# Kernel optimization log

Hardware: AMD Instinct MI355X
Metric: run time of the kernel (lower is better)

Reference implementation:

```python
import jax, jax.numpy as jnp
import numpy as np

GAMMA = 1.0 - 2.0 ** (-5)   # 0.96875, as in the module
NUM_GROUPS = 8
NUM_HEADS = 8
EPS = 1e-5


def setup_inputs() -> dict:
    key = jax.random.key(0)
    ks = jax.random.split(key, 8)
    M, S, Hd = 128, 512, 512  # num_segments, bonds per segment, hidden_size
    N = M * S
    return {
        "message": jax.random.normal(ks[0], (N, Hd), jnp.float32),
        "Wq": jax.random.normal(ks[1], (Hd, Hd), jnp.float32) / np.sqrt(Hd).astype(np.float32),
        "Wk": jax.random.normal(ks[2], (Hd, Hd), jnp.float32) / np.sqrt(Hd).astype(np.float32),
        "Wv": jax.random.normal(ks[3], (Hd, Hd), jnp.float32) / np.sqrt(Hd).astype(np.float32),
        "Wo": jax.random.normal(ks[4], (Hd, Hd), jnp.float32) / np.sqrt(Hd).astype(np.float32),
        "bo": jax.random.normal(ks[5], (Hd,), jnp.float32) * 0.01,
        "gn_w": jnp.ones((Hd,), jnp.float32),
        "gn_b": jnp.zeros((Hd,), jnp.float32),
        "num_segs": M,
        "seg_len": S,
    }


def _forward(message, Wq, Wk, Wv, Wo, bo, gn_w, gn_b, M, S):
    Hd = message.shape[1]
    H = NUM_HEADS
    d = Hd // H
    scale = jnp.float32(d ** (-0.5))
    gamma = jnp.float32(GAMMA)

    x = message.reshape(M, S, Hd)                       # equal contiguous segments
    q = (x @ Wq.T).reshape(M, S, H, d)
    k = (x @ Wk.T).reshape(M, S, H, d)
    v = (x @ Wv.T).reshape(M, S, H, d)

    # per-segment K^T V outer-product state contribution: [M, H, d, d]
    A = jnp.einsum('mshd,mshe->mhde', k, v)
    decay = gamma ** S  # gamma ** b_size for equal segments

    def step(r, a):
        # r = K_i^T V_i + gamma^{b_size} * r_prev  (state AFTER segment i, as in source)
        r_new = a + decay * r
        return r_new, r_new

    _, r_all = jax.lax.scan(step, jnp.zeros((H, d, d), x.dtype), A)  # [M, H, d, d]

    # intra-segment retention: (Q K^T) * scale @ V
    scores = jnp.einsum('mshd,mthd->mhst', q, k) * scale
    intra = jnp.einsum('mhst,mthd->mshd', scores, v)
    # cross/recurrent term: (Q @ r_i) * gamma^{i+1}  (note: NOT scaled by scale_factor)
    cross = jnp.einsum('mshd,mhde->mshe', q, r_all)
    g = (gamma ** jnp.arange(1, M + 1, dtype=jnp.float32))[:, None, None, None]
    h = jax.nn.relu(intra + cross * g)                  # activation; dropout p=0

    out = h.reshape(M, S, Hd) @ Wo.T + bo               # W_b_o
    res = x + out                                       # residual (dropout p=0)

    # GroupNorm(8, hidden): per segment (batch N=1), groups over hidden channels,
    # stats pooled over (hidden/8 group channels x S bonds)
    gsh = res.reshape(M, S, NUM_GROUPS, Hd // NUM_GROUPS)
    mean = gsh.mean(axis=(1, 3), keepdims=True)
    var = gsh.var(axis=(1, 3), keepdims=True)
    normed = ((gsh - mean) * jax.lax.rsqrt(var + EPS)).reshape(M, S, Hd)
    normed = normed * gn_w + gn_b

    flat = normed.reshape(M * S, Hd)
    # cached_zero_vector is prepended once before the first segment
    return jnp.concatenate([jnp.zeros((1, Hd), flat.dtype), flat], axis=0)


def reference(message, Wq, Wk, Wv, Wo, bo, gn_w, gn_b, num_segs, seg_len):
    return _forward(message, Wq, Wk, Wv, Wo, bo, gn_w, gn_b, num_segs, seg_len)
```

## Files before the change

kernel.cpp:

```cpp
#include <hip/hip_runtime.h>
#include <math.h>

#define M_SEG 128
#define S_SEG 512
#define HD 512
#define NHEAD 8
#define DHEAD 64
#define NROWS (M_SEG * S_SEG)
#define QKVLD 1536
#define GAMMA_F 0.96875f
#define SCALE_F 0.125f

typedef unsigned short u16;
typedef float f32x4 __attribute__((ext_vector_type(4)));
typedef __bf16 bf16x8 __attribute__((ext_vector_type(8)));
typedef unsigned short ushort8 __attribute__((ext_vector_type(8)));
typedef unsigned short ushort4v __attribute__((ext_vector_type(4)));

__device__ __forceinline__ u16 f2bf(float f) {
    union { float f; unsigned u; } x; x.f = f;
    unsigned r = x.u + 0x7FFFu + ((x.u >> 16) & 1u);
    return (u16)(r >> 16);
}
__device__ __forceinline__ float bf2f(u16 v) {
    union { unsigned u; float f; } x; x.u = ((unsigned)v) << 16;
    return x.f;
}

__device__ __forceinline__ void fence_all() {
    asm volatile("" ::: "memory");
    __builtin_amdgcn_sched_barrier(0);
}

__device__ __forceinline__ void gload16(const u16* g, u16* l) {
    __builtin_amdgcn_global_load_lds(
        (const __attribute__((address_space(1))) void*)g,
        (__attribute__((address_space(3))) void*)l, 16, 0, 0);
}

__global__ __launch_bounds__(256) void convert_bf16(const float* __restrict__ in,
                                                    u16* __restrict__ outp, int n8)
{
    int idx = blockIdx.x * 256 + threadIdx.x;
    if (idx >= n8) return;
    const float4 a = *reinterpret_cast<const float4*>(&in[(size_t)idx * 8]);
    const float4 b = *reinterpret_cast<const float4*>(&in[(size_t)idx * 8 + 4]);
    ushort8 o;
    o[0] = f2bf(a.x); o[1] = f2bf(a.y); o[2] = f2bf(a.z); o[3] = f2bf(a.w);
    o[4] = f2bf(b.x); o[5] = f2bf(b.y); o[6] = f2bf(b.z); o[7] = f2bf(b.w);
    *reinterpret_cast<ushort8*>(&outp[(size_t)idx * 8]) = o;
}

__global__ __launch_bounds__(256) void convert_weights(const float* __restrict__ w0,
                                                       const float* __restrict__ w1,
                                                       const float* __restrict__ w2,
                                                       const float* __restrict__ w3,
                                                       u16* __restrict__ outp)
{
    const int which = blockIdx.y;
    const float* src = which == 0 ? w0 : which == 1 ? w1 : which == 2 ? w2 : w3;
    u16* dst = outp + (size_t)which * 262144;
    int idx = blockIdx.x * 256 + threadIdx.x;
    const float4 a = *reinterpret_cast<const float4*>(&src[(size_t)idx * 8]);
    const float4 b = *reinterpret_cast<const float4*>(&src[(size_t)idx * 8 + 4]);
    ushort8 o;
    o[0] = f2bf(a.x); o[1] = f2bf(a.y); o[2] = f2bf(a.z); o[3] = f2bf(a.w);
    o[4] = f2bf(b.x); o[5] = f2bf(b.y); o[6] = f2bf(b.z); o[7] = f2bf(b.w);
    *reinterpret_cast<ushort8*>(&dst[(size_t)idx * 8]) = o;
}

template<int EPI>
__global__ __launch_bounds__(256, 4) void gemm4b(const u16* __restrict__ A, int lda,
                                                 const u16* __restrict__ B,
                                                 u16* __restrict__ Cv, int ldc, int ntile,
                                                 const u16* __restrict__ Xb,
                                                 const float* __restrict__ bias)
{
    __shared__ __align__(16) u16 sm[2][8192];
    const int t    = threadIdx.x;
    const int lane = t & 63;
    const int w    = t >> 6;
    const int wm   = w >> 1;
    const int wn   = w & 1;

    const int nwg  = gridDim.x;
    const int cpx  = nwg >> 3;
    const int bid  = blockIdx.x;
    const int sbid = (bid & 7) * cpx + (bid >> 3);
    const int mt = sbid / ntile, nt = sbid % ntile;
    const int rowBase = mt * 128, colBase = nt * 128;

    const int frow = lane & 15, fkc = lane >> 4, orow = (lane >> 4) * 4;

    const int sr0 = t >> 2;
    const int ksl = (t & 3) ^ ((sr0 >> 1) & 3);

    const size_t gA0 = (size_t)(rowBase + sr0)      * lda + ksl * 8;
    const size_t gA1 = (size_t)(rowBase + sr0 + 64) * lda + ksl * 8;
    const size_t gB0 = (size_t)(colBase + sr0)      * HD  + ksl * 8;
    const size_t gB1 = (size_t)(colBase + sr0 + 64) * HD  + ksl * 8;

    f32x4 acc[4][4];
#pragma unroll
    for (int i = 0; i < 4; ++i)
#pragma unroll
        for (int j = 0; j < 4; ++j)
            acc[i][j] = (f32x4){0.f, 0.f, 0.f, 0.f};

#define STAGE(kt, buf)                                                        \
    do {                                                                      \
        gload16(&A[gA0 + (kt) * 32], &sm[buf][t * 8]);                        \
        gload16(&A[gA1 + (kt) * 32], &sm[buf][2048 + t * 8]);                 \
        gload16(&B[gB0 + (kt) * 32], &sm[buf][4096 + t * 8]);                 \
        gload16(&B[gB1 + (kt) * 32], &sm[buf][6144 + t * 8]);                 \
    } while (0)

    STAGE(0, 0);
    STAGE(1, 1);

#pragma unroll 1
    for (int kt = 0; kt < 16; ++kt) {
        const int buf = kt & 1;
        if (kt < 15) asm volatile("s_waitcnt vmcnt(4)" ::: "memory");
        else         asm volatile("s_waitcnt vmcnt(0)" ::: "memory");
        __builtin_amdgcn_s_barrier();
        fence_all();

        const u16* Ab = sm[buf];
        const u16* Bb = sm[buf] + 4096;
        bf16x8 af[4], bfv[4];
#pragma unroll
        for (int mm = 0; mm < 4; ++mm) {
            const int r = wm * 64 + mm * 16 + frow;
            af[mm] = *reinterpret_cast<const bf16x8*>(
                &Ab[r * 32 + ((fkc ^ ((r >> 1) & 3)) << 3)]);
        }
#pragma unroll
        for (int nn = 0; nn < 4; ++nn) {
            const int r = wn * 64 + nn * 16 + frow;
            bfv[nn] = *reinterpret_cast<const bf16x8*>(
                &Bb[r * 32 + ((fkc ^ ((r >> 1) & 3)) << 3)]);
        }
        __builtin_amdgcn_s_setprio(1);
#pragma unroll
        for (int mm = 0; mm < 4; ++mm)
#pragma unroll
            for (int nn = 0; nn < 4; ++nn)
                acc[mm][nn] = __builtin_amdgcn_mfma_f32_16x16x32_bf16(af[mm], bfv[nn], acc[mm][nn], 0, 0, 0);
        __builtin_amdgcn_s_setprio(0);

        __builtin_amdgcn_s_barrier();
        fence_all();
        if (kt < 14) STAGE(kt + 2, buf);
    }
#undef STAGE

    if (EPI == 0) {
        u16* ldsC = (u16*)sm;
#pragma unroll
        for (int mm = 0; mm < 4; ++mm)
#pragma unroll
            for (int nn = 0; nn < 4; ++nn) {
                const int row0 = wm * 64 + mm * 16 + orow;
                const int col  = wn * 64 + nn * 16 + frow;
#pragma unroll
                for (int r = 0; r < 4; ++r)
                    ldsC[(row0 + r) * 128 + col] = f2bf(acc[mm][nn][r]);
            }
        __syncthreads();
#pragma unroll
        for (int p = 0; p < 8; ++p) {
            const int lin = p * 256 + t;
            const int row = lin >> 4, c8 = lin & 15;
            *reinterpret_cast<ushort8*>(
                &Cv[(size_t)(rowBase + row) * ldc + colBase + c8 * 8]) =
                *reinterpret_cast<const ushort8*>(&ldsC[row * 128 + c8 * 8]);
        }
    } else {
        float* ldsF = (float*)sm;
#pragma unroll
        for (int half = 0; half < 2; ++half) {
            __syncthreads();
            if (wm == half) {
#pragma unroll
                for (int mm = 0; mm < 4; ++mm)
#pragma unroll
                    for (int nn = 0; nn < 4; ++nn) {
                        const int row0 = mm * 16 + orow;
                        const int col  = wn * 64 + nn * 16 + frow;
#pragma unroll
                        for (int r = 0; r < 4; ++r)
                            ldsF[(row0 + r) * 128 + col] = acc[mm][nn][r];
                    }
            }
            __syncthreads();
#pragma unroll
            for (int p = 0; p < 8; ++p) {
                const int lin = p * 256 + t;
                const int row = lin >> 5, c4 = lin & 31;
                const int grow = rowBase + half * 64 + row;
                float4 a = *reinterpret_cast<const float4*>(&ldsF[row * 128 + c4 * 4]);
                ushort4v x4 = *reinterpret_cast<const ushort4v*>(
                    &Xb[(size_t)grow * HD + colBase + c4 * 4]);
                float4 b = *reinterpret_cast<const float4*>(&bias[colBase + c4 * 4]);
                ushort4v o;
                o[0] = f2bf(a.x + bf2f(x4[0]) + b.x);
                o[1] = f2bf(a.y + bf2f(x4[1]) + b.y);
                o[2] = f2bf(a.z + bf2f(x4[2]) + b.z);
                o[3] = f2bf(a.w + bf2f(x4[3]) + b.w);
                *reinterpret_cast<ushort4v*>(
                    &Cv[(size_t)grow * ldc + colBase + c4 * 4]) = o;
            }
        }
    }
}

__global__ __launch_bounds__(256) void kv_outer_mfma(const u16* __restrict__ qkv,
                                                     float* __restrict__ Abuf)
{
    __shared__ __align__(16) u16 kT[2048];
    __shared__ __align__(16) u16 vT[2048];
    const int t    = threadIdx.x;
    const int lane = t & 63;
    const int w    = t >> 6;
    const int hh   = blockIdx.x;
    const int m    = blockIdx.y;
    const int sl   = t & 31;
    const int dg   = (t >> 5) * 8;
    const int frow = lane & 15, fkc = lane >> 4, orow = (lane >> 4) * 4;
    const size_t gbase = (size_t)(m * S_SEG) * QKVLD + 512 + hh * DHEAD + dg;

    f32x4 acc[4];
#pragma unroll
    for (int i = 0; i < 4; ++i) acc[i] = (f32x4){0.f, 0.f, 0.f, 0.f};

    ushort8 ka, va, kb, vb;

#define LOADC(c, K8, V8)                                                      \
    do {                                                                      \
        size_t g_ = gbase + (size_t)((c) * 32 + sl) * QKVLD;                  \
        K8 = *reinterpret_cast<const ushort8*>(&qkv[g_]);                     \
        V8 = *reinterpret_cast<const ushort8*>(&qkv[g_ + 512]);               \
    } while (0)
#define WRTC(K8, V8)                                                          \
    do {                                                                      \
        _Pragma("unroll")                                                     \
        for (int j = 0; j < 8; ++j) {                                         \
            const int d_ = dg + j;                                            \
            const int a_ = d_ * 32 + ((((sl >> 3) ^ ((d_ >> 1) & 3))) << 3) + (sl & 7); \
            kT[a_] = K8[j];                                                   \
            vT[a_] = V8[j];                                                   \
        }                                                                     \
    } while (0)
#define CMPC()                                                                \
    do {                                                                      \
        bf16x8 kf[4], vf;                                                     \
        _Pragma("unroll")                                                     \
        for (int mf = 0; mf < 4; ++mf) {                                      \
            const int d_ = mf * 16 + frow;                                    \
            kf[mf] = *reinterpret_cast<const bf16x8*>(                        \
                &kT[d_ * 32 + ((fkc ^ ((d_ >> 1) & 3)) << 3)]);               \
        }                                                                     \
        const int e_ = w * 16 + frow;                                         \
        vf = *reinterpret_cast<const bf16x8*>(                                \
            &vT[e_ * 32 + ((fkc ^ ((e_ >> 1) & 3)) << 3)]);                   \
        _Pragma("unroll")                                                     \
        for (int mf = 0; mf < 4; ++mf)                                        \
            acc[mf] = __builtin_amdgcn_mfma_f32_16x16x32_bf16(kf[mf], vf, acc[mf], 0, 0, 0); \
    } while (0)

    LOADC(0, ka, va);
#pragma unroll 1
    for (int cc = 0; cc < 16; cc += 2) {
        WRTC(ka, va);
        LOADC(cc + 1, kb, vb);
        asm volatile("s_waitcnt lgkmcnt(0)" ::: "memory");
        __builtin_amdgcn_s_barrier();
        __builtin_amdgcn_sched_barrier(0);
        CMPC();
        __builtin_amdgcn_s_barrier();
        fence_all();

        WRTC(kb, vb);
        if (cc + 2 < 16) LOADC(cc + 2, ka, va);
        asm volatile("s_waitcnt lgkmcnt(0)" ::: "memory");
        __builtin_amdgcn_s_barrier();
        __builtin_amdgcn_sched_barrier(0);
        CMPC();
        __builtin_amdgcn_s_barrier();
        fence_all();
    }
#undef LOADC
#undef WRTC
#undef CMPC

    const size_t hb = (size_t)(m * NHEAD + hh) * DHEAD * DHEAD;
#pragma unroll
    for (int mf = 0; mf < 4; ++mf)
#pragma unroll
        for (int r = 0; r < 4; ++r)
            Abuf[hb + (size_t)(mf * 16 + orow + r) * DHEAD + w * 16 + frow] = acc[mf][r];
}

__global__ __launch_bounds__(256) void scan_kernel(const float* __restrict__ Abuf,
                                                   float* __restrict__ Bc)
{
    const int tid = blockIdx.x * 256 + threadIdx.x;
    const float decay = powf(GAMMA_F, (float)S_SEG);
    float r = 0.0f;
    float g = 1.0f;
    for (int m = 0; m < M_SEG; ++m) {
        float a = Abuf[(size_t)m * 32768 + tid];
        r = fmaf(decay, r, a);
        g *= GAMMA_F;
        Bc[(size_t)m * 32768 + tid] = fmaf(g, r, SCALE_F * a);
    }
}

__global__ __launch_bounds__(256) void h_mfma(u16* __restrict__ qkv,
                                              const float* __restrict__ Bc)
{
    __shared__ __align__(16) u16 BT[64 * 72];
    const int t    = threadIdx.x;
    const int lane = t & 63;
    const int w    = t >> 6;
    const int m    = blockIdx.y;
    const int sBase = blockIdx.x * 256 + w * 64;
    const int frow = lane & 15;
    const int fkc  = lane >> 4;

    for (int hh = 0; hh < NHEAD; ++hh) {
#pragma unroll
        for (int i = 0; i < 4; ++i) {
            int idx = t + i * 256;
            int d = idx >> 4, e4 = idx & 15;
            float4 v = *reinterpret_cast<const float4*>(
                &Bc[((size_t)(m * NHEAD + hh) * DHEAD + d) * DHEAD + e4 * 4]);
            BT[(e4 * 4 + 0) * 72 + d] = f2bf(v.x);
            BT[(e4 * 4 + 1) * 72 + d] = f2bf(v.y);
            BT[(e4 * 4 + 2) * 72 + d] = f2bf(v.z);
            BT[(e4 * 4 + 3) * 72 + d] = f2bf(v.w);
        }
        __syncthreads();

        f32x4 acc[4][4];
#pragma unroll
        for (int i = 0; i < 4; ++i)
#pragma unroll
            for (int j = 0; j < 4; ++j)
                acc[i][j] = (f32x4){0.f, 0.f, 0.f, 0.f};

#pragma unroll
        for (int ks = 0; ks < 2; ++ks) {
            bf16x8 af[4], bfr[4];
#pragma unroll
            for (int mm = 0; mm < 4; ++mm) {
                const int grow = m * S_SEG + sBase + mm * 16 + frow;
                af[mm] = *reinterpret_cast<const bf16x8*>(
                    &qkv[(size_t)grow * QKVLD + hh * DHEAD + ks * 32 + fkc * 8]);
                const int e = mm * 16 + frow;
                bfr[mm] = *reinterpret_cast<const bf16x8*>(&BT[e * 72 + ks * 32 + fkc * 8]);
            }
#pragma unroll
            for (int mm = 0; mm < 4; ++mm)
#pragma unroll
                for (int nn = 0; nn < 4; ++nn)
                    acc[mm][nn] = __builtin_amdgcn_mfma_f32_16x16x32_bf16(af[mm], bfr[nn], acc[mm][nn], 0, 0, 0);
        }

        const int orow = (lane >> 4) * 4;
#pragma unroll
        for (int mm = 0; mm < 4; ++mm)
#pragma unroll
            for (int nn = 0; nn < 4; ++nn) {
                const int col  = hh * DHEAD + nn * 16 + frow;
                const int row0 = m * S_SEG + sBase + mm * 16 + orow;
#pragma unroll
                for (int r = 0; r < 4; ++r)
                    qkv[(size_t)(row0 + r) * QKVLD + col] = f2bf(fmaxf(acc[mm][nn][r], 0.f));
            }
        __syncthreads();
    }
}

__global__ __launch_bounds__(256) void groupnorm_bf16(const u16* __restrict__ res,
                                                      float* __restrict__ out,
                                                      const float* __restrict__ gn_w,
                                                      const float* __restrict__ gn_b)
{
    const int g = blockIdx.x;
    const int m = blockIdx.y;
    const int t = threadIdx.x;
    const u16* base = res + (size_t)(m * S_SEG) * QKVLD + g * DHEAD;

    float sum = 0.0f, sq = 0.0f;
    for (int idx = t; idx < 4096; idx += 256) {
        int s = idx >> 3, c8 = idx & 7;
        ushort8 v = *reinterpret_cast<const ushort8*>(&base[(size_t)s * QKVLD + c8 * 8]);
#pragma unroll
        for (int j = 0; j < 8; ++j) {
            float f = bf2f(v[j]);
            sum += f; sq += f * f;
        }
    }
    __shared__ float rs[256], rq[256];
    rs[t] = sum; rq[t] = sq;
    __syncthreads();
    for (int off = 128; off > 0; off >>= 1) {
        if (t < off) { rs[t] += rs[t + off]; rq[t] += rq[t + off]; }
        __syncthreads();
    }
    __shared__ float smean, sinv;
    if (t == 0) {
        float mean = rs[0] * (1.0f / 32768.0f);
        float var  = rq[0] * (1.0f / 32768.0f) - mean * mean;
        smean = mean;
        sinv  = rsqrtf(var + 1e-5f);
    }
    __syncthreads();
    const float mean = smean, inv = sinv;

    for (int idx = t; idx < 4096; idx += 256) {
        int s = idx >> 3, c8 = idx & 7;
        ushort8 v = *reinterpret_cast<const ushort8*>(&base[(size_t)s * QKVLD + c8 * 8]);
        float o[8];
#pragma unroll
        for (int j = 0; j < 8; ++j) {
            float wj = gn_w[g * DHEAD + c8 * 8 + j];
            float bj = gn_b[g * DHEAD + c8 * 8 + j];
            o[j] = (bf2f(v[j]) - mean) * inv * wj + bj;
        }
        float* dst = &out[(size_t)(1 + m * S_SEG + s) * HD + g * DHEAD + c8 * 8];
        *reinterpret_cast<float4*>(dst)     = make_float4(o[0], o[1], o[2], o[3]);
        *reinterpret_cast<float4*>(dst + 4) = make_float4(o[4], o[5], o[6], o[7]);
    }
}

__global__ void zero_row(float* __restrict__ out)
{
    int i = blockIdx.x * 256 + threadIdx.x;
    if (i < HD) out[i] = 0.0f;
}

extern "C" void kernel_launch(void* const* d_in, const int* in_sizes, int n_in,
                              void* d_out, int out_size, void* d_ws, size_t ws_size,
                              hipStream_t stream)
{
    const float* msg = (const float*)d_in[0];
    const float* Wq  = (const float*)d_in[1];
    const float* Wk  = (const float*)d_in[2];
    const float* Wv  = (const float*)d_in[3];
    const float* Wo  = (const float*)d_in[4];
    const float* bo  = (const float*)d_in[5];
    const float* gnw = (const float*)d_in[6];
    const float* gnb = (const float*)d_in[7];
    float* out = (float*)d_out;

    u16*   msgb = (u16*)out;
    float* Abuf = out + 16777216;
    float* Bc   = out + 16777216 + 4194304;

    u16* Wb   = (u16*)d_ws;
    u16* qkv  = Wb + 4 * 262144;
    u16* resB = qkv + 512;

    convert_weights<<<dim3(128, 4), 256, 0, stream>>>(Wq, Wk, Wv, Wo, Wb);
    convert_bf16<<<16384, 256, 0, stream>>>(msg, msgb, 4194304);

    gemm4b<0><<<6144, 256, 0, stream>>>(msgb, HD, Wb, qkv, QKVLD, 12, nullptr, nullptr);

    kv_outer_mfma<<<dim3(NHEAD, M_SEG), 256, 0, stream>>>(qkv, Abuf);
    scan_kernel<<<128, 256, 0, stream>>>(Abuf, Bc);
    h_mfma<<<dim3(2, M_SEG), 256, 0, stream>>>(qkv, Bc);

    gemm4b<1><<<2048, 256, 0, stream>>>(qkv, QKVLD, Wb + 3 * 262144, resB, QKVLD, 4, msgb, bo);

    zero_row<<<2, 256, 0, stream>>>(out);
    groupnorm_bf16<<<dim3(8, M_SEG), 256, 0, stream>>>(resB, out, gnw, gnb);
}
```

Baseline: 374.3 us.

## Merge conversion kernels, stage h stores via LDS, cache groupnorm tile in LDS

```diff
diff --git a/kernel.cpp b/kernel.cpp
--- a/kernel.cpp
+++ b/kernel.cpp
@@ -38,34 +38,32 @@
         (__attribute__((address_space(3))) void*)l, 16, 0, 0);
 }
 
-__global__ __launch_bounds__(256) void convert_bf16(const float* __restrict__ in,
-                                                    u16* __restrict__ outp, int n8)
-{
-    int idx = blockIdx.x * 256 + threadIdx.x;
-    if (idx >= n8) return;
-    const float4 a = *reinterpret_cast<const float4*>(&in[(size_t)idx * 8]);
-    const float4 b = *reinterpret_cast<const float4*>(&in[(size_t)idx * 8 + 4]);
+__global__ __launch_bounds__(256) void convert_all(const float* __restrict__ msg,
+                                                   const float* __restrict__ w0,
+                                                   const float* __restrict__ w1,
+                                                   const float* __restrict__ w2,
+                                                   const float* __restrict__ w3,
+                                                   u16* __restrict__ msgb,
+                                                   u16* __restrict__ Wb)
+{
+    const int b = blockIdx.x;
+    const float* src;
+    u16* dst;
+    int idx;
+    if (b < 16384) {
+        src = msg; dst = msgb; idx = b * 256 + threadIdx.x;
+    } else {
+        const int wb = b - 16384;
+        const int which = wb >> 7;
+        src = which == 0 ? w0 : which == 1 ? w1 : which == 2 ? w2 : w3;
+        dst = Wb + (size_t)which * 262144;
+        idx = (wb & 127) * 256 + threadIdx.x;
+    }
+    const float4 a = *reinterpret_cast<const float4*>(&src[(size_t)idx * 8]);
+    const float4 c = *reinterpret_cast<const float4*>(&src[(size_t)idx * 8 + 4]);
     ushort8 o;
     o[0] = f2bf(a.x); o[1] = f2bf(a.y); o[2] = f2bf(a.z); o[3] = f2bf(a.w);
-    o[4] = f2bf(b.x); o[5] = f2bf(b.y); o[6] = f2bf(b.z); o[7] = f2bf(b.w);
-    *reinterpret_cast<ushort8*>(&outp[(size_t)idx * 8]) = o;
-}
-
-__global__ __launch_bounds__(256) void convert_weights(const float* __restrict__ w0,
-                                                       const float* __restrict__ w1,
-                                                       const float* __restrict__ w2,
-                                                       const float* __restrict__ w3,
-                                                       u16* __restrict__ outp)
-{
-    const int which = blockIdx.y;
-    const float* src = which == 0 ? w0 : which == 1 ? w1 : which == 2 ? w2 : w3;
-    u16* dst = outp + (size_t)which * 262144;
-    int idx = blockIdx.x * 256 + threadIdx.x;
-    const float4 a = *reinterpret_cast<const float4*>(&src[(size_t)idx * 8]);
-    const float4 b = *reinterpret_cast<const float4*>(&src[(size_t)idx * 8 + 4]);
-    ushort8 o;
-    o[0] = f2bf(a.x); o[1] = f2bf(a.y); o[2] = f2bf(a.z); o[3] = f2bf(a.w);
-    o[4] = f2bf(b.x); o[5] = f2bf(b.y); o[6] = f2bf(b.z); o[7] = f2bf(b.w);
+    o[4] = f2bf(c.x); o[5] = f2bf(c.y); o[6] = f2bf(c.z); o[7] = f2bf(c.w);
     *reinterpret_cast<ushort8*>(&dst[(size_t)idx * 8]) = o;
 }
 
@@ -321,13 +319,16 @@
                                               const float* __restrict__ Bc)
 {
     __shared__ __align__(16) u16 BT[64 * 72];
+    __shared__ __align__(16) u16 hC[256 * 68];
     const int t    = threadIdx.x;
     const int lane = t & 63;
     const int w    = t >> 6;
     const int m    = blockIdx.y;
-    const int sBase = blockIdx.x * 256 + w * 64;
+    const int bRow0 = blockIdx.x * 256;
+    const int sBase = bRow0 + w * 64;
     const int frow = lane & 15;
     const int fkc  = lane >> 4;
+    const int orow = (lane >> 4) * 4;
 
     for (int hh = 0; hh < NHEAD; ++hh) {
 #pragma unroll
@@ -368,17 +369,25 @@
                     acc[mm][nn] = __builtin_amdgcn_mfma_f32_16x16x32_bf16(af[mm], bfr[nn], acc[mm][nn], 0, 0, 0);
         }
 
-        const int orow = (lane >> 4) * 4;
 #pragma unroll
         for (int mm = 0; mm < 4; ++mm)
 #pragma unroll
             for (int nn = 0; nn < 4; ++nn) {
-                const int col  = hh * DHEAD + nn * 16 + frow;
-                const int row0 = m * S_SEG + sBase + mm * 16 + orow;
+                const int rl0 = w * 64 + mm * 16 + orow;
+                const int cl  = nn * 16 + frow;
 #pragma unroll
                 for (int r = 0; r < 4; ++r)
-                    qkv[(size_t)(row0 + r) * QKVLD + col] = f2bf(fmaxf(acc[mm][nn][r], 0.f));
+                    hC[(rl0 + r) * 68 + cl] = f2bf(fmaxf(acc[mm][nn][r], 0.f));
             }
+        __syncthreads();
+#pragma unroll
+        for (int i = 0; i < 8; ++i) {
+            const int lin = i * 256 + t;
+            const int row = lin >> 3, c8 = lin & 7;
+            *reinterpret_cast<ushort8*>(
+                &qkv[(size_t)(m * S_SEG + bRow0 + row) * QKVLD + hh * DHEAD + c8 * 8]) =
+                *reinterpret_cast<const ushort8*>(&hC[row * 68 + c8 * 8]);
+        }
         __syncthreads();
     }
 }
@@ -388,15 +397,19 @@
                                                       const float* __restrict__ gn_w,
                                                       const float* __restrict__ gn_b)
 {
+    __shared__ __align__(16) u16 hL[512 * 64];
     const int g = blockIdx.x;
     const int m = blockIdx.y;
     const int t = threadIdx.x;
     const u16* base = res + (size_t)(m * S_SEG) * QKVLD + g * DHEAD;
 
+    if (m == 0 && t < 64) out[g * DHEAD + t] = 0.0f;
+
     float sum = 0.0f, sq = 0.0f;
     for (int idx = t; idx < 4096; idx += 256) {
         int s = idx >> 3, c8 = idx & 7;
         ushort8 v = *reinterpret_cast<const ushort8*>(&base[(size_t)s * QKVLD + c8 * 8]);
+        *reinterpret_cast<ushort8*>(&hL[s * 64 + c8 * 8]) = v;
 #pragma unroll
         for (int j = 0; j < 8; ++j) {
             float f = bf2f(v[j]);
@@ -422,7 +435,7 @@
 
     for (int idx = t; idx < 4096; idx += 256) {
         int s = idx >> 3, c8 = idx & 7;
-        ushort8 v = *reinterpret_cast<const ushort8*>(&base[(size_t)s * QKVLD + c8 * 8]);
+        ushort8 v = *reinterpret_cast<const ushort8*>(&hL[s * 64 + c8 * 8]);
         float o[8];
 #pragma unroll
         for (int j = 0; j < 8; ++j) {
@@ -434,12 +447,6 @@
         *reinterpret_cast<float4*>(dst)     = make_float4(o[0], o[1], o[2], o[3]);
         *reinterpret_cast<float4*>(dst + 4) = make_float4(o[4], o[5], o[6], o[7]);
     }
-}
-
-__global__ void zero_row(float* __restrict__ out)
-{
-    int i = blockIdx.x * 256 + threadIdx.x;
-    if (i < HD) out[i] = 0.0f;
 }
 
 extern "C" void kernel_launch(void* const* d_in, const int* in_sizes, int n_in,
@@ -464,8 +471,7 @@
     u16* qkv  = Wb + 4 * 262144;
     u16* resB = qkv + 512;
 
-    convert_weights<<<dim3(128, 4), 256, 0, stream>>>(Wq, Wk, Wv, Wo, Wb);
-    convert_bf16<<<16384, 256, 0, stream>>>(msg, msgb, 4194304);
+    convert_all<<<16896, 256, 0, stream>>>(msg, Wq, Wk, Wv, Wo, msgb, Wb);
 
     gemm4b<0><<<6144, 256, 0, stream>>>(msgb, HD, Wb, qkv, QKVLD, 12, nullptr, nullptr);
 
@@ -475,6 +481,5 @@
 
     gemm4b<1><<<2048, 256, 0, stream>>>(qkv, QKVLD, Wb + 3 * 262144, resB, QKVLD, 4, msgb, bo);
 
-    zero_row<<<2, 256, 0, stream>>>(out);
     groupnorm_bf16<<<dim3(8, M_SEG), 256, 0, stream>>>(resB, out, gnw, gnb);
 }
```

After: 360.4 us (median of 2 runs). -3.7%, faster.
